# Kernel tuning notes

Measured on AMD Instinct MI355X. Metric: run time of the kernel, lower is better.

The kernel has to match this reference:

```python
import jax, jax.numpy as jnp
import numpy as np

H = 8        # num_heads
L = 2        # num_layers
F = 9        # num_fields
D = 128      # n_field_info
DH = D       # per-head depth = (D*H)//H
NB = 50      # n_base
EXCL = (0, 1, 2)  # fields excluded in FinalMerge (SelfAttention_Ex0, n_fields-3 inputs)
EPS = 1e-5


def _ln(x, g, b):
    m = jnp.mean(x, -1, keepdims=True)
    v = jnp.mean((x - m) ** 2, -1, keepdims=True)
    return (x - m) / jnp.sqrt(v + EPS) * g + b


def _forward(Y, Gin, posW1, posB1, posW2, posB2, posW3, posB3,
             Wq, bq, Wk, bk, Wv, bv, Wo, bo, lnG, lnB, fnG, fnB, poolW,
             uQW, uQB, uKW, uKB, uVW, uVB, mQW, mQB, mKW, mKB, mVW, mVB):
    B, S, _ = Y.shape
    pooled = []
    for f in range(F):  # per-field towers are structurally distinct (separate params)
        gy = jnp.concatenate([Y, Gin[:, :, f:f + 1]], axis=-1)        # [B,S,NB+1]
        h = jnp.tanh(gy @ posW1[f].T + posB1[f])
        h = jnp.tanh(h @ posW2[f].T + posB2[f])
        x = jax.nn.sigmoid(h @ posW3[f].T + posB3[f])                  # [B,S,D]
        for l in range(L):
            q = (x @ Wq[l, f].T + bq[l, f]).reshape(B, S, H, DH).transpose(0, 2, 1, 3)
            k = (x @ Wk[l, f].T + bk[l, f]).reshape(B, S, H, DH).transpose(0, 2, 1, 3)
            v = (x @ Wv[l, f].T + bv[l, f]).reshape(B, S, H, DH).transpose(0, 2, 1, 3)
            att = jax.nn.softmax(jnp.einsum('bhsd,bhtd->bhst', q, k) / jnp.sqrt(jnp.float32(DH)), axis=-1)
            wv = jnp.einsum('bhst,bhtd->bhsd', att, v).transpose(0, 2, 1, 3).reshape(B, S, H * DH)
            out = wv @ Wo[l, f].T + bo[l, f]
            x = _ln(x + out, lnG[l, f], lnB[l, f])   # residual + per-field LayerNorm
        x = _ln(x, fnG, fnB)                         # final_norm
        sc = jax.nn.softmax(x @ poolW[f][:, None], axis=1)             # GlobalAttentionPooling, [B,S,1]
        pooled.append(jnp.sum(x * sc, axis=1))                         # [B,D]
    U = jnp.stack(pooled, axis=-1)                                     # [B,D,F]

    unified = []
    for f in range(F):  # SelfAttention per target field
        Q = U @ uQW[f].T + uQB[f]                                      # [B,D,D]
        K = U @ uKW[f].T + uKB[f]
        V = U @ uVW[f].T + uVB[f]
        A = jax.nn.softmax(jnp.einsum('bik,bjk->bij', Q, K) / jnp.sqrt(jnp.float32(F)), axis=-1)
        o = jnp.einsum('bij,bjk->bik', A, V).mean(axis=-1)             # [B,D]
        o = o + (U[:, :, f] if f > 0 else U.mean(axis=-1))
        unified.append(o)
    Uu = jnp.stack(unified, axis=-1)                                   # [B,D,F]

    inc = [i for i in range(F) if i not in EXCL]
    Us = U[:, :, jnp.array(inc)]                                       # [B,D,F-3]
    Q = Us @ mQW.T + mQB
    K = Us @ mKW.T + mKB
    V = Us @ mVW.T + mVB
    A = jax.nn.softmax(jnp.einsum('bik,bjk->bij', Q, K) / jnp.sqrt(jnp.float32(F)), axis=-1)
    g = jnp.einsum('bij,bjk->bik', A, V).mean(axis=-1) + Us.mean(axis=-1)  # [B,D]
    return jnp.concatenate([Uu, g[:, :, None]], axis=-1)               # [B,D,F+1]


def setup_inputs() -> dict:
    key = jax.random.key(0)
    ks = iter(jax.random.split(key, 64))
    nrm = lambda shape, s=1.0: jax.random.normal(next(ks), shape, dtype=jnp.float32) * s
    B, S = 8, 512
    d = {}
    d['Y'] = nrm((B, S, NB))
    d['Gin'] = nrm((B, S, F))
    d['posW1'] = nrm((F, 50, NB + 1), 0.14); d['posB1'] = jnp.zeros((F, 50))
    d['posW2'] = nrm((F, 50, 50), 0.14);     d['posB2'] = jnp.zeros((F, 50))
    d['posW3'] = nrm((F, D, 50), 0.14);      d['posB3'] = jnp.zeros((F, D))
    d['Wq'] = nrm((L, F, H * DH, D), 0.09);  d['bq'] = jnp.zeros((L, F, H * DH))
    d['Wk'] = nrm((L, F, H * DH, D), 0.09);  d['bk'] = jnp.zeros((L, F, H * DH))
    d['Wv'] = nrm((L, F, H * DH, D), 0.09);  d['bv'] = jnp.zeros((L, F, H * DH))
    d['Wo'] = nrm((L, F, D, H * DH), 0.03);  d['bo'] = jnp.zeros((L, F, D))
    d['lnG'] = jnp.ones((L, F, D)); d['lnB'] = jnp.zeros((L, F, D))
    d['fnG'] = jnp.ones((D,));      d['fnB'] = jnp.zeros((D,))
    d['poolW'] = nrm((F, D))
    d['uQW'] = nrm((F, D, F), 0.33); d['uQB'] = jnp.zeros((F, D))
    d['uKW'] = nrm((F, D, F), 0.33); d['uKB'] = jnp.zeros((F, D))
    d['uVW'] = nrm((F, D, F), 0.33); d['uVB'] = jnp.zeros((F, D))
    d['mQW'] = nrm((D, F - 3), 0.4); d['mQB'] = jnp.zeros((D,))
    d['mKW'] = nrm((D, F - 3), 0.4); d['mKB'] = jnp.zeros((D,))
    d['mVW'] = nrm((D, F - 3), 0.4); d['mVB'] = jnp.zeros((D,))
    return d


def reference(Y, Gin, posW1, posB1, posW2, posB2, posW3, posB3,
              Wq, bq, Wk, bk, Wv, bv, Wo, bo, lnG, lnB, fnG, fnB, poolW,
              uQW, uQB, uKW, uKB, uVW, uVB, mQW, mQB, mKW, mKB, mVW, mVB):
    return _forward(Y, Gin, posW1, posB1, posW2, posB2, posW3, posB3,
                    Wq, bq, Wk, bk, Wv, bv, Wo, bo, lnG, lnB, fnG, fnB, poolW,
                    uQW, uQB, uKW, uKB, uVW, uVB, mQW, mQB, mKW, mKB, mVW, mVB)
```

## Files before the change

### kernel.cpp

```cpp
#include <hip/hip_runtime.h>
#include <hip/hip_bf16.h>

#define F_  9
#define B_  8
#define S_  512
#define H_  8
#define DH_ 128
#define D_  128
#define NB_ 50
#define BS_ 4096
#define PERBUF 4194304UL
#define WELEMS 2359296UL

typedef short bf16x8 __attribute__((ext_vector_type(8)));
typedef float f32x4  __attribute__((ext_vector_type(4)));
typedef unsigned int u32x4 __attribute__((ext_vector_type(4)));

static __device__ __forceinline__ unsigned short f2b(float f) {
    unsigned int u = __float_as_uint(f);
    unsigned int r = (u + 0x7FFFu + ((u >> 16) & 1u)) >> 16;
    return (unsigned short)r;
}
static __device__ __forceinline__ float b2f(unsigned short u) {
    return __uint_as_float(((unsigned int)u) << 16);
}
static __device__ __forceinline__ unsigned int cvtpk(float lo, float hi) {
    unsigned int r;
    asm("v_cvt_pk_bf16_f32 %0, %1, %2" : "=v"(r) : "v"(lo), "v"(hi));
    return r;
}

__global__ __launch_bounds__(256) void cvt_kernel(
    const float* __restrict__ in, unsigned short* __restrict__ out, int n)
{
    int i = (blockIdx.x * 256 + threadIdx.x) * 8;
    if (i + 8 <= n) {
        float4 a = *(const float4*)&in[i];
        float4 b = *(const float4*)&in[i + 4];
        ushort4 o0 = { f2b(a.x), f2b(a.y), f2b(a.z), f2b(a.w) };
        ushort4 o1 = { f2b(b.x), f2b(b.y), f2b(b.z), f2b(b.w) };
        *(ushort4*)&out[i]     = o0;
        *(ushort4*)&out[i + 4] = o1;
    }
}

__global__ __launch_bounds__(256) void posnet_kernel(
    const float* __restrict__ Y, const float* __restrict__ Gin,
    const float* __restrict__ W1g, const float* __restrict__ B1,
    const float* __restrict__ W2g, const float* __restrict__ B2,
    const float* __restrict__ W3g, const float* __restrict__ B3,
    float* __restrict__ xA, unsigned short* __restrict__ xAb)
{
    __shared__ float w1[50*51];
    __shared__ float w2[50*50];
    __shared__ float w3[128*50];
    __shared__ float b1[64], b2[64], b3[128];
    int f = blockIdx.z;
    int t = threadIdx.x;
    for (int i = t; i < 2550; i += 256) w1[i] = W1g[f*2550 + i];
    for (int i = t; i < 2500; i += 256) w2[i] = W2g[f*2500 + i];
    for (int i = t; i < 6400; i += 256) w3[i] = W3g[f*6400 + i];
    if (t < 50) { b1[t] = B1[f*50 + t]; b2[t] = B2[f*50 + t]; }
    if (t < 128) b3[t] = B3[f*128 + t];
    __syncthreads();

    int lane = t & 63, w = t >> 6;
    int row = blockIdx.x * 4 + w;

    float gy = 0.f;
    if (lane < 50)       gy = Y[(size_t)row*50 + lane];
    else if (lane == 50) gy = Gin[(size_t)row*F_ + f];

    float a1 = (lane < 50) ? b1[lane] : 0.f;
    for (int kk = 0; kk < 51; ++kk) {
        float g = __shfl(gy, kk);
        if (lane < 50) a1 += w1[lane*51 + kk] * g;
    }
    float h1 = tanhf(a1);

    float a2 = (lane < 50) ? b2[lane] : 0.f;
    for (int kk = 0; kk < 50; ++kk) {
        float hh = __shfl(h1, kk);
        if (lane < 50) a2 += w2[lane*50 + kk] * hh;
    }
    float h2 = tanhf(a2);

    float a30 = b3[lane], a31 = b3[64 + lane];
    for (int kk = 0; kk < 50; ++kk) {
        float hh = __shfl(h2, kk);
        a30 += w3[lane*50 + kk] * hh;
        a31 += w3[(64 + lane)*50 + kk] * hh;
    }
    float s0v = 1.f / (1.f + expf(-a30));
    float s1v = 1.f / (1.f + expf(-a31));
    size_t roff = ((size_t)f*BS_ + row)*128;
    xA[roff + lane]       = s0v;
    xA[roff + 64 + lane]  = s1v;
    xAb[roff + lane]      = f2b(s0v);
    xAb[roff + 64 + lane] = f2b(s1v);
}

__global__ __launch_bounds__(256) void qkv_mfma_kernel(
    const unsigned short* __restrict__ xb,
    const unsigned short* __restrict__ Wqb, const unsigned short* __restrict__ Wkb,
    const unsigned short* __restrict__ Wvb,
    const float* __restrict__ bq, const float* __restrict__ bk, const float* __restrict__ bv,
    unsigned short* __restrict__ qo, unsigned short* __restrict__ ko,
    unsigned int* __restrict__ vto, int l, int f0)
{
    int z = blockIdx.z;
    int fl = z / 3, which = z - fl*3;
    int f = f0 + fl;
    const unsigned short* W; const float* bias;
    if (which == 0)      { W = Wqb; bias = bq; }
    else if (which == 1) { W = Wkb; bias = bk; }
    else                 { W = Wvb; bias = bv; }
    W    += (size_t)(l*F_ + f) * 1024 * 128;
    bias += (size_t)(l*F_ + f) * 1024;

    int m0 = blockIdx.x * 128;
    int n0 = blockIdx.y * 128;
    int t = threadIdx.x, w = t >> 6, ln = t & 63, g = ln >> 4, c = ln & 15;
    int wr = w >> 1, wc = w & 1;

    const unsigned short* Ab = xb + ((size_t)f*BS_ + m0 + wr*64)*128;
    const unsigned short* Bb = W + (size_t)(n0 + wc*64)*128;

    f32x4 acc[4][4];
#pragma unroll
    for (int mi = 0; mi < 4; ++mi)
#pragma unroll
        for (int ni = 0; ni < 4; ++ni) acc[mi][ni] = (f32x4){0.f,0.f,0.f,0.f};

#pragma unroll
    for (int kt = 0; kt < 4; ++kt) {
        bf16x8 af[4], bfr[4];
#pragma unroll
        for (int mi = 0; mi < 4; ++mi)
            af[mi] = *(const bf16x8*)&Ab[(size_t)(mi*16 + c)*128 + kt*32 + g*8];
#pragma unroll
        for (int ni = 0; ni < 4; ++ni)
            bfr[ni] = *(const bf16x8*)&Bb[(size_t)(ni*16 + c)*128 + kt*32 + g*8];
#pragma unroll
        for (int mi = 0; mi < 4; ++mi)
#pragma unroll
            for (int ni = 0; ni < 4; ++ni)
                acc[mi][ni] = __builtin_amdgcn_mfma_f32_16x16x32_bf16(af[mi], bfr[ni], acc[mi][ni], 0, 0, 0);
    }

    int h = n0 >> 7;
    float bs_[4];
#pragma unroll
    for (int ni = 0; ni < 4; ++ni) bs_[ni] = bias[n0 + wc*64 + ni*16 + c];

    if (which < 2) {
        float qscale = (which == 0) ? 0.08838834764831845f : 1.0f;
        unsigned short* out = (which == 0 ? qo : ko) + (size_t)fl * PERBUF;
#pragma unroll
        for (int mi = 0; mi < 4; ++mi) {
#pragma unroll
            for (int r = 0; r < 4; ++r) {
                int m = m0 + wr*64 + mi*16 + 4*g + r;
                int b = m >> 9, s = m & 511;
                unsigned short* orow = out + (((size_t)(b*H_ + h))*S_ + s)*128;
#pragma unroll
                for (int ni = 0; ni < 4; ++ni)
                    orow[wc*64 + ni*16 + c] = f2b((acc[mi][ni][r] + bs_[ni]) * qscale);
            }
        }
    } else {
        unsigned int* vtf = vto + (size_t)fl * (PERBUF/2);
#pragma unroll
        for (int mi = 0; mi < 4; ++mi) {
            int mbase = m0 + wr*64 + mi*16 + 4*g;
            int b = mbase >> 9, sh = (mbase & 511) >> 1;
            unsigned int* vtp = vtf + ((size_t)(b*H_ + h))*32768;
#pragma unroll
            for (int ni = 0; ni < 4; ++ni) {
                int d = wc*64 + ni*16 + c;
                float bb_ = bs_[ni];
                unsigned int p01 = (unsigned int)f2b(acc[mi][ni][0] + bb_)
                                 | ((unsigned int)f2b(acc[mi][ni][1] + bb_) << 16);
                unsigned int p23 = (unsigned int)f2b(acc[mi][ni][2] + bb_)
                                 | ((unsigned int)f2b(acc[mi][ni][3] + bb_) << 16);
                vtp[(size_t)d*256 + sh]     = p01;
                vtp[(size_t)d*256 + sh + 1] = p23;
            }
        }
    }
}

__global__ __launch_bounds__(256) void attn_mfma_kernel(
    const unsigned short* __restrict__ q, const unsigned short* __restrict__ k,
    const unsigned int* __restrict__ vt, unsigned short* __restrict__ wv)
{
    int t = threadIdx.x;
    int w = t >> 6, ln = t & 63, g = ln >> 4, c = ln & 15;
    int bid = blockIdx.x;
    int group = bid >> 5, within = bid & 31;
    int i = within >> 3, hl = within & 7;
    int hIdx = group*8 + hl;
    int fl = hIdx >> 6, by = hIdx & 63;
    int q0 = i*128 + w*32;

    const unsigned short* qh = q + ((size_t)(fl*64 + by))*S_*128;
    const unsigned short* kh = k + ((size_t)(fl*64 + by))*S_*128;
    const unsigned int*  vth = vt + ((size_t)(fl*64 + by))*32768;
    int b = by >> 3, h = by & 7;
    unsigned short* wvh = wv + ((size_t)(fl*B_ + b))*S_*1024 + h*128;

    __shared__ alignas(16) unsigned short Ks[2][32][136];
    __shared__ alignas(16) unsigned int   Vs[2][128][20];

    int krow = t >> 4, kseg = t & 15;
    int vrow = t >> 2, vseg = t & 3;

    bf16x8 qf[2][4];
#pragma unroll
    for (int gq = 0; gq < 2; ++gq)
#pragma unroll
        for (int d0 = 0; d0 < 4; ++d0)
            qf[gq][d0] = *(const bf16x8*)&qh[(size_t)(q0 + gq*16 + c)*128 + d0*32 + g*8];

    f32x4 acc[2][8];
#pragma unroll
    for (int gq = 0; gq < 2; ++gq)
#pragma unroll
        for (int i2 = 0; i2 < 8; ++i2) acc[gq][i2] = (f32x4){0.f, 0.f, 0.f, 0.f};
    float mrow[2] = {-1e30f, -1e30f};
    float lrow[2] = {0.f, 0.f};

    int srcA = ((g & 1) << 5) + c;
    int srcB = srcA + 16;
    bool glow = (g < 2);

    uint4 kr0, kr1, vr0, vr1;
    {
        kr0 = *(const uint4*)&kh[(size_t)krow*128 + kseg*8];
        kr1 = *(const uint4*)&kh[(size_t)(krow + 16)*128 + kseg*8];
        vr0 = *(const uint4*)&vth[(size_t)vrow*256 + vseg*4];
        vr1 = *(const uint4*)&vth[(size_t)(vrow + 64)*256 + vseg*4];
        *(uint4*)&Ks[0][krow][kseg*8]      = kr0;
        *(uint4*)&Ks[0][krow + 16][kseg*8] = kr1;
        *(uint4*)&Vs[0][vrow][vseg*4]      = vr0;
        *(uint4*)&Vs[0][vrow + 64][vseg*4] = vr1;
    }
    __syncthreads();

    int cur = 0;
    for (int kt = 0; kt < 16; ++kt) {
        if (kt < 15) {
            const unsigned short* ks = kh + (size_t)(kt + 1)*32*128;
            const unsigned int*  vsp = vth + (kt + 1)*16;
            kr0 = *(const uint4*)&ks[(size_t)krow*128 + kseg*8];
            kr1 = *(const uint4*)&ks[(size_t)(krow + 16)*128 + kseg*8];
            vr0 = *(const uint4*)&vsp[(size_t)vrow*256 + vseg*4];
            vr1 = *(const uint4*)&vsp[(size_t)(vrow + 64)*256 + vseg*4];
        }

        f32x4 s[2][2];
        s[0][0] = (f32x4){0.f,0.f,0.f,0.f}; s[0][1] = (f32x4){0.f,0.f,0.f,0.f};
        s[1][0] = (f32x4){0.f,0.f,0.f,0.f}; s[1][1] = (f32x4){0.f,0.f,0.f,0.f};
        __builtin_amdgcn_s_setprio(1);
#pragma unroll
        for (int d0 = 0; d0 < 4; ++d0) {
            bf16x8 k0 = *(const bf16x8*)&Ks[cur][c][g*8 + d0*32];
            bf16x8 k1 = *(const bf16x8*)&Ks[cur][16 + c][g*8 + d0*32];
#pragma unroll
            for (int gq = 0; gq < 2; ++gq) {
                s[gq][0] = __builtin_amdgcn_mfma_f32_16x16x32_bf16(k0, qf[gq][d0], s[gq][0], 0, 0, 0);
                s[gq][1] = __builtin_amdgcn_mfma_f32_16x16x32_bf16(k1, qf[gq][d0], s[gq][1], 0, 0, 0);
            }
        }
        __builtin_amdgcn_s_setprio(0);

        float corr[2];
        bf16x8 pa[2];
        bool need = false;
#pragma unroll
        for (int gq = 0; gq < 2; ++gq) {
            float t0 = fmaxf(fmaxf(fmaxf(s[gq][0][0], s[gq][0][1]), fmaxf(s[gq][0][2], s[gq][0][3])),
                             fmaxf(fmaxf(s[gq][1][0], s[gq][1][1]), fmaxf(s[gq][1][2], s[gq][1][3])));
            t0 = fmaxf(t0, __shfl_xor(t0, 16));
            t0 = fmaxf(t0, __shfl_xor(t0, 32));
            float mo = mrow[gq];
            float mn = (t0 > mo + 8.f) ? t0 : mo;
            float co = __expf(mo - mn);
            corr[gq] = co;
            mrow[gq] = mn;
            float p00 = __expf(s[gq][0][0] - mn), p01 = __expf(s[gq][0][1] - mn);
            float p02 = __expf(s[gq][0][2] - mn), p03 = __expf(s[gq][0][3] - mn);
            float p10 = __expf(s[gq][1][0] - mn), p11 = __expf(s[gq][1][1] - mn);
            float p12 = __expf(s[gq][1][2] - mn), p13 = __expf(s[gq][1][3] - mn);
            float ps = ((p00 + p01) + (p02 + p03)) + ((p10 + p11) + (p12 + p13));
            ps += __shfl_xor(ps, 16);
            ps += __shfl_xor(ps, 32);
            lrow[gq] = lrow[gq]*co + ps;
            need = need || (co != 1.0f);

            unsigned int pk0 = cvtpk(p00, p01), pk1 = cvtpk(p02, p03);
            unsigned int pk2 = cvtpk(p10, p11), pk3 = cvtpk(p12, p13);
            unsigned int a0 = __shfl(pk0, srcA), a1 = __shfl(pk1, srcA);
            unsigned int b0 = __shfl(pk0, srcB), b1 = __shfl(pk1, srcB);
            unsigned int c0 = __shfl(pk2, srcA), c1 = __shfl(pk3, srcA);
            unsigned int d0_ = __shfl(pk2, srcB), d1_ = __shfl(pk3, srcB);
            u32x4 pu;
            pu[0] = glow ? a0 : c0;
            pu[1] = glow ? a1 : c1;
            pu[2] = glow ? b0 : d0_;
            pu[3] = glow ? b1 : d1_;
            pa[gq] = __builtin_bit_cast(bf16x8, pu);
        }

        if (__any(need)) {
#pragma unroll
            for (int gq = 0; gq < 2; ++gq) {
                float cr0 = __shfl(corr[gq], 4*g + 0);
                float cr1 = __shfl(corr[gq], 4*g + 1);
                float cr2 = __shfl(corr[gq], 4*g + 2);
                float cr3 = __shfl(corr[gq], 4*g + 3);
#pragma unroll
                for (int i2 = 0; i2 < 8; ++i2) {
                    f32x4 a = acc[gq][i2];
                    a[0] *= cr0; a[1] *= cr1; a[2] *= cr2; a[3] *= cr3;
                    acc[gq][i2] = a;
                }
            }
        }

        __builtin_amdgcn_s_setprio(1);
#pragma unroll
        for (int i2 = 0; i2 < 8; ++i2) {
            bf16x8 vf = *(const bf16x8*)&Vs[cur][i2*16 + c][g*4];
            acc[0][i2] = __builtin_amdgcn_mfma_f32_16x16x32_bf16(pa[0], vf, acc[0][i2], 0, 0, 0);
            acc[1][i2] = __builtin_amdgcn_mfma_f32_16x16x32_bf16(pa[1], vf, acc[1][i2], 0, 0, 0);
        }
        __builtin_amdgcn_s_setprio(0);

        if (kt < 15) {
            __syncthreads();
            int nxt = cur ^ 1;
            *(uint4*)&Ks[nxt][krow][kseg*8]      = kr0;
            *(uint4*)&Ks[nxt][krow + 16][kseg*8] = kr1;
            *(uint4*)&Vs[nxt][vrow][vseg*4]      = vr0;
            *(uint4*)&Vs[nxt][vrow + 64][vseg*4] = vr1;
            __syncthreads();
            cur = nxt;
        }
    }

#pragma unroll
    for (int gq = 0; gq < 2; ++gq) {
        float invq = 1.0f / lrow[gq];
        float iv0 = __shfl(invq, 4*g + 0);
        float iv1 = __shfl(invq, 4*g + 1);
        float iv2 = __shfl(invq, 4*g + 2);
        float iv3 = __shfl(invq, 4*g + 3);
#pragma unroll
        for (int i2 = 0; i2 < 8; ++i2) {
            unsigned short* wp = &wvh[(size_t)(q0 + gq*16 + 4*g)*1024 + i2*16 + c];
            wp[0]    = f2b(acc[gq][i2][0]*iv0);
            wp[1024] = f2b(acc[gq][i2][1]*iv1);
            wp[2048] = f2b(acc[gq][i2][2]*iv2);
            wp[3072] = f2b(acc[gq][i2][3]*iv3);
        }
    }
}

__global__ __launch_bounds__(256) void outproj_mfma_kernel(
    const unsigned short* __restrict__ wv, const unsigned short* __restrict__ Wob,
    const float* __restrict__ bo, const float* __restrict__ xin,
    float* __restrict__ xout, int l, int f0)
{
    int fl = blockIdx.z, f = f0 + fl;
    int m0 = blockIdx.x * 128;
    int t = threadIdx.x, w = t >> 6, ln = t & 63, g = ln >> 4, c = ln & 15;
    int wr = w >> 1, wc = w & 1;

    const unsigned short* Ab = wv + ((size_t)fl*BS_ + m0 + wr*64)*1024;
    const unsigned short* Bb = Wob + (size_t)(l*F_ + f)*128*1024 + (size_t)(wc*64)*1024;
    const float* bob = bo + (size_t)(l*F_ + f)*128;

    f32x4 acc[4][4];
#pragma unroll
    for (int mi = 0; mi < 4; ++mi)
#pragma unroll
        for (int ni = 0; ni < 4; ++ni) acc[mi][ni] = (f32x4){0.f,0.f,0.f,0.f};

#pragma unroll 4
    for (int kt = 0; kt < 32; ++kt) {
        bf16x8 af[4], bfr[4];
#pragma unroll
        for (int mi = 0; mi < 4; ++mi)
            af[mi] = *(const bf16x8*)&Ab[(size_t)(mi*16 + c)*1024 + kt*32 + g*8];
#pragma unroll
        for (int ni = 0; ni < 4; ++ni)
            bfr[ni] = *(const bf16x8*)&Bb[(size_t)(ni*16 + c)*1024 + kt*32 + g*8];
#pragma unroll
        for (int mi = 0; mi < 4; ++mi)
#pragma unroll
            for (int ni = 0; ni < 4; ++ni)
                acc[mi][ni] = __builtin_amdgcn_mfma_f32_16x16x32_bf16(af[mi], bfr[ni], acc[mi][ni], 0, 0, 0);
    }

    float bs_[4];
#pragma unroll
    for (int ni = 0; ni < 4; ++ni) bs_[ni] = bob[wc*64 + ni*16 + c];

#pragma unroll
    for (int mi = 0; mi < 4; ++mi) {
#pragma unroll
        for (int r = 0; r < 4; ++r) {
            int m = m0 + wr*64 + mi*16 + 4*g + r;
            const float* xr = xin + ((size_t)f*BS_ + m)*128;
            float* xo = xout + ((size_t)f*BS_ + m)*128;
#pragma unroll
            for (int ni = 0; ni < 4; ++ni) {
                int n = wc*64 + ni*16 + c;
                xo[n] = acc[mi][ni][r] + bs_[ni] + xr[n];
            }
        }
    }
}

__global__ __launch_bounds__(256) void ln_kernel(
    const float* __restrict__ xin, float* __restrict__ xout,
    unsigned short* __restrict__ xoutb,
    const float* __restrict__ g, const float* __restrict__ bb, int f0, int gstride)
{
    int t = threadIdx.x, lane = t & 63, w = t >> 6;
    int rowl = blockIdx.x * 4 + w;
    int fl = rowl >> 12;
    size_t row = (size_t)f0*BS_ + rowl;
    const float* xi = xin + row*128;
    float a = xi[lane], c = xi[64 + lane];
    float s = a + c;
#pragma unroll
    for (int off = 1; off < 64; off <<= 1) s += __shfl_xor(s, off);
    float mean = s * (1.0f/128.0f);
    float da = a - mean, dc = c - mean;
    float vs = da*da + dc*dc;
#pragma unroll
    for (int off = 1; off < 64; off <<= 1) vs += __shfl_xor(vs, off);
    float inv = rsqrtf(vs * (1.0f/128.0f) + 1e-5f);
    const float* gp = g + (size_t)fl*gstride;
    const float* bp = bb + (size_t)fl*gstride;
    float o0 = da*inv*gp[lane]      + bp[lane];
    float o1 = dc*inv*gp[64 + lane] + bp[64 + lane];
    float* xo = xout + row*128;
    xo[lane]      = o0;
    xo[64 + lane] = o1;
    xoutb[row*128 + lane]      = f2b(o0);
    xoutb[row*128 + 64 + lane] = f2b(o1);
}

__global__ __launch_bounds__(256) void pool_kernel(
    const float* __restrict__ xB, const float* __restrict__ poolW,
    float* __restrict__ U, int f0)
{
    int f = f0 + blockIdx.x, b = blockIdx.y;
    const float* xb = xB + ((size_t)f*BS_ + (size_t)b*S_)*128;
    const float* pw = poolW + f*128;
    __shared__ float sc[512];
    __shared__ float red[8];
    __shared__ float MS[2];
    __shared__ float pool2[256];
    int t = threadIdx.x, lane = t & 63, w = t >> 6;

    float p0 = pw[lane], p1 = pw[64 + lane];
    for (int s = w; s < 512; s += 4) {
        float a = xb[(size_t)s*128 + lane]*p0 + xb[(size_t)s*128 + 64 + lane]*p1;
#pragma unroll
        for (int off = 1; off < 64; off <<= 1) a += __shfl_xor(a, off);
        if (lane == 0) sc[s] = a;
    }
    __syncthreads();

    float m = -1e30f;
    for (int s = t; s < 512; s += 256) m = fmaxf(m, sc[s]);
#pragma unroll
    for (int off = 1; off < 64; off <<= 1) m = fmaxf(m, __shfl_xor(m, off));
    if (lane == 0) red[w] = m;
    __syncthreads();
    if (t == 0) MS[0] = fmaxf(fmaxf(red[0], red[1]), fmaxf(red[2], red[3]));
    __syncthreads();
    float M = MS[0];

    float ssum = 0.f;
    for (int s = t; s < 512; s += 256) { float e = expf(sc[s] - M); sc[s] = e; ssum += e; }
#pragma unroll
    for (int off = 1; off < 64; off <<= 1) ssum += __shfl_xor(ssum, off);
    if (lane == 0) red[4 + w] = ssum;
    __syncthreads();
    if (t == 0) MS[1] = red[4] + red[5] + red[6] + red[7];
    __syncthreads();
    float inv = 1.0f / MS[1];

    int d = t & 127, hh = t >> 7;
    float a = 0.f;
    for (int s = hh*256; s < hh*256 + 256; ++s) a += sc[s]*xb[(size_t)s*128 + d];
    pool2[t] = a;
    __syncthreads();
    if (t < 128) U[((size_t)b*128 + d)*F_ + f] = (pool2[t] + pool2[t + 128]) * inv;
}

__global__ __launch_bounds__(256) void unified_kernel(
    const float* __restrict__ U,
    const float* __restrict__ uQW, const float* __restrict__ uQB,
    const float* __restrict__ uKW, const float* __restrict__ uKB,
    const float* __restrict__ uVW, const float* __restrict__ uVB,
    float* __restrict__ outp)
{
    int f = blockIdx.x, b = blockIdx.y;
    __shared__ float Ub[128*9];
    __shared__ float Wj[128*9];
    __shared__ float zj[128];
    __shared__ float vm[128];
    __shared__ float Mm[81];
    __shared__ float wvm[9], bvec[9];
    __shared__ float cc_[2];
    int t = threadIdx.x;
    for (int i = t; i < 1152; i += 256) Ub[i] = U[(size_t)b*1152 + i];
    const float* qw = uQW + (size_t)f*1152;
    const float* kw = uKW + (size_t)f*1152;
    const float* vw = uVW + (size_t)f*1152;
    const float* qb = uQB + (size_t)f*128;
    const float* kb = uKB + (size_t)f*128;
    const float* vb = uVB + (size_t)f*128;

    if (t < 81) {
        int t1 = t/9, s1 = t%9; float a = 0.f;
        for (int kk = 0; kk < 128; ++kk) a += qw[kk*9 + t1]*kw[kk*9 + s1];
        Mm[t] = a;
    } else if (t < 90) {
        int s1 = t - 81; float a = 0.f;
        for (int kk = 0; kk < 128; ++kk) a += kw[kk*9 + s1]*qb[kk];
        bvec[s1] = a;
    } else if (t < 99) {
        int t1 = t - 90; float a = 0.f;
        for (int kk = 0; kk < 128; ++kk) a += vw[kk*9 + t1];
        wvm[t1] = a * (1.0f/128.0f);
    } else if (t == 99) {
        float a = 0.f, c2 = 0.f;
        for (int kk = 0; kk < 128; ++kk) { a += qb[kk]*kb[kk]; c2 += vb[kk]; }
        cc_[0] = a; cc_[1] = c2 * (1.0f/128.0f);
    }
    __syncthreads();

    if (t < 128) {
        int j = t;
        for (int t1 = 0; t1 < 9; ++t1) {
            float a = 0.f;
            for (int s1 = 0; s1 < 9; ++s1) a += Mm[t1*9 + s1]*Ub[j*9 + s1];
            Wj[j*9 + t1] = a;
        }
        float z = cc_[0], v2 = cc_[1];
        for (int s1 = 0; s1 < 9; ++s1) { z += bvec[s1]*Ub[j*9 + s1]; v2 += wvm[s1]*Ub[j*9 + s1]; }
        zj[j] = z; vm[j] = v2;
    }
    __syncthreads();

    int i = t >> 1, half = t & 1;
    float ui[9];
#pragma unroll
    for (int s1 = 0; s1 < 9; ++s1) ui[s1] = Ub[i*9 + s1];

    float mx = -1e30f;
    for (int jj = 0; jj < 64; ++jj) {
        int j = half*64 + jj;
        float a = zj[j];
#pragma unroll
        for (int s1 = 0; s1 < 9; ++s1) a += ui[s1]*Wj[j*9 + s1];
        mx = fmaxf(mx, a * (1.0f/3.0f));
    }
    mx = fmaxf(mx, __shfl_xor(mx, 1));
    float sum = 0.f, o = 0.f;
    for (int jj = 0; jj < 64; ++jj) {
        int j = half*64 + jj;
        float a = zj[j];
#pragma unroll
        for (int s1 = 0; s1 < 9; ++s1) a += ui[s1]*Wj[j*9 + s1];
        float p = expf(a * (1.0f/3.0f) - mx);
        sum += p; o += p*vm[j];
    }
    sum += __shfl_xor(sum, 1);
    o   += __shfl_xor(o, 1);
    if (half == 0) {
        float base;
        if (f > 0) base = ui[f];
        else { base = 0.f; for (int s1 = 0; s1 < 9; ++s1) base += ui[s1]; base *= (1.0f/9.0f); }
        outp[((size_t)b*128 + i)*10 + f] = o/sum + base;
    }
}

__global__ __launch_bounds__(256) void merge_kernel(
    const float* __restrict__ U,
    const float* __restrict__ mQW, const float* __restrict__ mQB,
    const float* __restrict__ mKW, const float* __restrict__ mKB,
    const float* __restrict__ mVW, const float* __restrict__ mVB,
    float* __restrict__ outp)
{
    int b = blockIdx.x;
    __shared__ float Us[128*6];
    __shared__ float Wj[128*6];
    __shared__ float zj[128];
    __shared__ float vm[128];
    __shared__ float Mm[36];
    __shared__ float wvm[6], bvec[6];
    __shared__ float cc_[2];
    int t = threadIdx.x;
    for (int i = t; i < 768; i += 256) {
        int j = i/6, tt = i - j*6;
        Us[i] = U[(size_t)b*1152 + j*9 + 3 + tt];
    }
    if (t < 36) {
        int t1 = t/6, s1 = t%6; float a = 0.f;
        for (int kk = 0; kk < 128; ++kk) a += mQW[kk*6 + t1]*mKW[kk*6 + s1];
        Mm[t] = a;
    } else if (t < 42) {
        int s1 = t - 36; float a = 0.f;
        for (int kk = 0; kk < 128; ++kk) a += mKW[kk*6 + s1]*mQB[kk];
        bvec[s1] = a;
    } else if (t < 48) {
        int t1 = t - 42; float a = 0.f;
        for (int kk = 0; kk < 128; ++kk) a += mVW[kk*6 + t1];
        wvm[t1] = a * (1.0f/128.0f);
    } else if (t == 48) {
        float a = 0.f, c2 = 0.f;
        for (int kk = 0; kk < 128; ++kk) { a += mQB[kk]*mKB[kk]; c2 += mVB[kk]; }
        cc_[0] = a; cc_[1] = c2 * (1.0f/128.0f);
    }
    __syncthreads();

    if (t < 128) {
        int j = t;
        for (int t1 = 0; t1 < 6; ++t1) {
            float a = 0.f;
            for (int s1 = 0; s1 < 6; ++s1) a += Mm[t1*6 + s1]*Us[j*6 + s1];
            Wj[j*6 + t1] = a;
        }
        float z = cc_[0], v2 = cc_[1];
        for (int s1 = 0; s1 < 6; ++s1) { z += bvec[s1]*Us[j*6 + s1]; v2 += wvm[s1]*Us[j*6 + s1]; }
        zj[j] = z; vm[j] = v2;
    }
    __syncthreads();

    int i = t >> 1, half = t & 1;
    float ui[6];
#pragma unroll
    for (int s1 = 0; s1 < 6; ++s1) ui[s1] = Us[i*6 + s1];

    float mx = -1e30f;
    for (int jj = 0; jj < 64; ++jj) {
        int j = half*64 + jj;
        float a = zj[j];
#pragma unroll
        for (int s1 = 0; s1 < 6; ++s1) a += ui[s1]*Wj[j*6 + s1];
        mx = fmaxf(mx, a * (1.0f/3.0f));
    }
    mx = fmaxf(mx, __shfl_xor(mx, 1));
    float sum = 0.f, o = 0.f;
    for (int jj = 0; jj < 64; ++jj) {
        int j = half*64 + jj;
        float a = zj[j];
#pragma unroll
        for (int s1 = 0; s1 < 6; ++s1) a += ui[s1]*Wj[j*6 + s1];
        float p = expf(a * (1.0f/3.0f) - mx);
        sum += p; o += p*vm[j];
    }
    sum += __shfl_xor(sum, 1);
    o   += __shfl_xor(o, 1);
    if (half == 0) {
        float base = 0.f;
        for (int s1 = 0; s1 < 6; ++s1) base += ui[s1];
        base *= (1.0f/6.0f);
        outp[((size_t)b*128 + i)*10 + 9] = o/sum + base;
    }
}

extern "C" void kernel_launch(void* const* d_in, const int* in_sizes, int n_in,
                              void* d_out, int out_size, void* d_ws, size_t ws_size,
                              hipStream_t stream)
{
    const float* Y     = (const float*)d_in[0];
    const float* Gin   = (const float*)d_in[1];
    const float* posW1 = (const float*)d_in[2];
    const float* posB1 = (const float*)d_in[3];
    const float* posW2 = (const float*)d_in[4];
    const float* posB2 = (const float*)d_in[5];
    const float* posW3 = (const float*)d_in[6];
    const float* posB3 = (const float*)d_in[7];
    const float* Wq    = (const float*)d_in[8];
    const float* bq    = (const float*)d_in[9];
    const float* Wk    = (const float*)d_in[10];
    const float* bk    = (const float*)d_in[11];
    const float* Wv    = (const float*)d_in[12];
    const float* bv    = (const float*)d_in[13];
    const float* Wo    = (const float*)d_in[14];
    const float* bo    = (const float*)d_in[15];
    const float* lnG   = (const float*)d_in[16];
    const float* lnB   = (const float*)d_in[17];
    const float* fnG   = (const float*)d_in[18];
    const float* fnB   = (const float*)d_in[19];
    const float* poolW = (const float*)d_in[20];
    const float* uQW   = (const float*)d_in[21];
    const float* uQB   = (const float*)d_in[22];
    const float* uKW   = (const float*)d_in[23];
    const float* uKB   = (const float*)d_in[24];
    const float* uVW   = (const float*)d_in[25];
    const float* uVB   = (const float*)d_in[26];
    const float* mQW   = (const float*)d_in[27];
    const float* mQB   = (const float*)d_in[28];
    const float* mKW   = (const float*)d_in[29];
    const float* mKB   = (const float*)d_in[30];
    const float* mVW   = (const float*)d_in[31];
    const float* mVB   = (const float*)d_in[32];

    const size_t xelems = (size_t)F_ * BS_ * 128;
    char* p = (char*)d_ws;
    float* xA   = (float*)p;               p += xelems*4;
    float* xB   = (float*)p;               p += xelems*4;
    float* Ubuf = (float*)p;               p += 16384*4;
    unsigned short* xAb = (unsigned short*)p; p += xelems*2;
    unsigned short* Wqb = (unsigned short*)p; p += WELEMS*2;
    unsigned short* Wkb = (unsigned short*)p; p += WELEMS*2;
    unsigned short* Wvb = (unsigned short*)p; p += WELEMS*2;
    unsigned short* Wob = (unsigned short*)p; p += WELEMS*2;
    size_t fixed_bytes = (size_t)(p - (char*)d_ws);

    size_t avail = (ws_size > fixed_bytes) ? (ws_size - fixed_bytes) : 0;
    size_t per_f = 8UL * PERBUF;
    int FC = (int)(avail / per_f);
    if (FC < 1) FC = 1;
    if (FC > F_) FC = F_;

    unsigned short* qb  = (unsigned short*)p;
    unsigned short* kb  = qb + (size_t)FC*PERBUF;
    unsigned short* wvb = kb + (size_t)FC*PERBUF;
    unsigned int*   vtb = (unsigned int*)(wvb + (size_t)FC*PERBUF);

    {
        int n = (int)WELEMS, grid = (n/8 + 255)/256;
        cvt_kernel<<<grid, 256, 0, stream>>>(Wq, Wqb, n);
        cvt_kernel<<<grid, 256, 0, stream>>>(Wk, Wkb, n);
        cvt_kernel<<<grid, 256, 0, stream>>>(Wv, Wvb, n);
        cvt_kernel<<<grid, 256, 0, stream>>>(Wo, Wob, n);
    }

    posnet_kernel<<<dim3(1024, 1, F_), 256, 0, stream>>>(
        Y, Gin, posW1, posB1, posW2, posB2, posW3, posB3, xA, xAb);

    for (int l = 0; l < 2; ++l) {
        for (int f0 = 0; f0 < F_; f0 += FC) {
            int fc = (F_ - f0) < FC ? (F_ - f0) : FC;
            qkv_mfma_kernel<<<dim3(32, 8, 3*fc), 256, 0, stream>>>(
                xAb, Wqb, Wkb, Wvb, bq, bk, bv, qb, kb, vtb, l, f0);
            attn_mfma_kernel<<<dim3(256*fc), 256, 0, stream>>>(qb, kb, vtb, wvb);
            outproj_mfma_kernel<<<dim3(32, 1, fc), 256, 0, stream>>>(
                wvb, Wob, bo, xA, xB, l, f0);
            ln_kernel<<<dim3(fc*1024), 256, 0, stream>>>(
                xB, xA, xAb, lnG + (size_t)(l*F_ + f0)*128, lnB + (size_t)(l*F_ + f0)*128, f0, 128);
        }
    }

    for (int f0 = 0; f0 < F_; f0 += FC) {
        int fc = (F_ - f0) < FC ? (F_ - f0) : FC;
        ln_kernel<<<dim3(fc*1024), 256, 0, stream>>>(xA, xB, xAb, fnG, fnB, f0, 0);
        pool_kernel<<<dim3(fc, 8), 256, 0, stream>>>(xB, poolW, Ubuf, f0);
    }

    unified_kernel<<<dim3(F_, B_), 256, 0, stream>>>(
        Ubuf, uQW, uQB, uKW, uKB, uVW, uVB, (float*)d_out);
    merge_kernel<<<dim3(B_), 256, 0, stream>>>(
        Ubuf, mQW, mQB, mKW, mKB, mVW, mVB, (float*)d_out);
}
```

Measured before the change: 1.174 ms.

## Restructure posnet to keep weights in registers and process 16 rows per wave

The position-net MLP now has each lane hold one weight row in registers and compute 16 rows per wave, with inputs staged in shared memory and read as float4. This replaces reloading every weight matrix into shared memory in each of 9216 tiny blocks, leaving 576 blocks with more reuse per weight. Separately, the four weight conversion launches are merged into one 2D-grid kernel to cut launch overhead. The register arrays (about 100 floats for the third layer plus accumulators) may raise register pressure and lower occupancy.

```diff
diff --git a/kernel.cpp b/kernel.cpp
--- a/kernel.cpp
+++ b/kernel.cpp
@@ -30,17 +30,27 @@
     return r;
 }
 
-__global__ __launch_bounds__(256) void cvt_kernel(
-    const float* __restrict__ in, unsigned short* __restrict__ out, int n)
-{
+__global__ __launch_bounds__(256) void cvt4_kernel(
+    const float* __restrict__ s0, const float* __restrict__ s1,
+    const float* __restrict__ s2, const float* __restrict__ s3,
+    unsigned short* __restrict__ d0, unsigned short* __restrict__ d1,
+    unsigned short* __restrict__ d2, unsigned short* __restrict__ d3, int n)
+{
+    const float* s; unsigned short* d;
+    switch (blockIdx.y) {
+        case 0: s = s0; d = d0; break;
+        case 1: s = s1; d = d1; break;
+        case 2: s = s2; d = d2; break;
+        default: s = s3; d = d3; break;
+    }
     int i = (blockIdx.x * 256 + threadIdx.x) * 8;
     if (i + 8 <= n) {
-        float4 a = *(const float4*)&in[i];
-        float4 b = *(const float4*)&in[i + 4];
+        float4 a = *(const float4*)&s[i];
+        float4 b = *(const float4*)&s[i + 4];
         ushort4 o0 = { f2b(a.x), f2b(a.y), f2b(a.z), f2b(a.w) };
         ushort4 o1 = { f2b(b.x), f2b(b.y), f2b(b.z), f2b(b.w) };
-        *(ushort4*)&out[i]     = o0;
-        *(ushort4*)&out[i + 4] = o1;
+        *(ushort4*)&d[i]     = o0;
+        *(ushort4*)&d[i + 4] = o1;
     }
 }
 
@@ -51,53 +61,112 @@
     const float* __restrict__ W3g, const float* __restrict__ B3,
     float* __restrict__ xA, unsigned short* __restrict__ xAb)
 {
-    __shared__ float w1[50*51];
-    __shared__ float w2[50*50];
-    __shared__ float w3[128*50];
-    __shared__ float b1[64], b2[64], b3[128];
-    int f = blockIdx.z;
-    int t = threadIdx.x;
-    for (int i = t; i < 2550; i += 256) w1[i] = W1g[f*2550 + i];
-    for (int i = t; i < 2500; i += 256) w2[i] = W2g[f*2500 + i];
-    for (int i = t; i < 6400; i += 256) w3[i] = W3g[f*6400 + i];
-    if (t < 50) { b1[t] = B1[f*50 + t]; b2[t] = B2[f*50 + t]; }
-    if (t < 128) b3[t] = B3[f*128 + t];
-    __syncthreads();
-
-    int lane = t & 63, w = t >> 6;
-    int row = blockIdx.x * 4 + w;
-
-    float gy = 0.f;
-    if (lane < 50)       gy = Y[(size_t)row*50 + lane];
-    else if (lane == 50) gy = Gin[(size_t)row*F_ + f];
-
-    float a1 = (lane < 50) ? b1[lane] : 0.f;
-    for (int kk = 0; kk < 51; ++kk) {
-        float g = __shfl(gy, kk);
-        if (lane < 50) a1 += w1[lane*51 + kk] * g;
-    }
-    float h1 = tanhf(a1);
-
-    float a2 = (lane < 50) ? b2[lane] : 0.f;
-    for (int kk = 0; kk < 50; ++kk) {
-        float hh = __shfl(h1, kk);
-        if (lane < 50) a2 += w2[lane*50 + kk] * hh;
-    }
-    float h2 = tanhf(a2);
-
-    float a30 = b3[lane], a31 = b3[64 + lane];
-    for (int kk = 0; kk < 50; ++kk) {
-        float hh = __shfl(h2, kk);
-        a30 += w3[lane*50 + kk] * hh;
-        a31 += w3[(64 + lane)*50 + kk] * hh;
-    }
-    float s0v = 1.f / (1.f + expf(-a30));
-    float s1v = 1.f / (1.f + expf(-a31));
-    size_t roff = ((size_t)f*BS_ + row)*128;
-    xA[roff + lane]       = s0v;
-    xA[roff + 64 + lane]  = s1v;
-    xAb[roff + lane]      = f2b(s0v);
-    xAb[roff + 64 + lane] = f2b(s1v);
+    __shared__ float gys[4][16][52];
+    __shared__ float hs[4][16][52];
+
+    int f = blockIdx.y;
+    int t = threadIdx.x, w = t >> 6, j = t & 63;
+    int rowbase = blockIdx.x * 64 + w * 16;
+
+#pragma unroll
+    for (int rr = 0; rr < 16; ++rr) {
+        int row = rowbase + rr;
+        if (j < 50)       gys[w][rr][j]  = Y[(size_t)row*50 + j];
+        else if (j == 50) gys[w][rr][50] = Gin[(size_t)row*F_ + f];
+    }
+
+    int jj = (j < 50) ? j : 0;
+    float acc0[16], acc1[16];
+
+    {
+        const float* wp = W1g + f*2550 + jj*51;
+        float wreg[51];
+#pragma unroll
+        for (int kk = 0; kk < 51; ++kk) wreg[kk] = wp[kk];
+        float bb = B1[f*50 + jj];
+#pragma unroll
+        for (int rr = 0; rr < 16; ++rr) acc0[rr] = bb;
+#pragma unroll
+        for (int k4 = 0; k4 < 48; k4 += 4) {
+#pragma unroll
+            for (int rr = 0; rr < 16; ++rr) {
+                float4 gv = *(const float4*)&gys[w][rr][k4];
+                acc0[rr] += wreg[k4]*gv.x + wreg[k4+1]*gv.y + wreg[k4+2]*gv.z + wreg[k4+3]*gv.w;
+            }
+        }
+#pragma unroll
+        for (int kk = 48; kk < 51; ++kk)
+#pragma unroll
+            for (int rr = 0; rr < 16; ++rr) acc0[rr] += wreg[kk]*gys[w][rr][kk];
+        if (j < 50) {
+#pragma unroll
+            for (int rr = 0; rr < 16; ++rr) hs[w][rr][j] = tanhf(acc0[rr]);
+        }
+    }
+
+    {
+        const float* wp = W2g + f*2500 + jj*50;
+        float wreg[50];
+#pragma unroll
+        for (int kk = 0; kk < 50; ++kk) wreg[kk] = wp[kk];
+        float bb = B2[f*50 + jj];
+#pragma unroll
+        for (int rr = 0; rr < 16; ++rr) acc0[rr] = bb;
+#pragma unroll
+        for (int k4 = 0; k4 < 48; k4 += 4) {
+#pragma unroll
+            for (int rr = 0; rr < 16; ++rr) {
+                float4 gv = *(const float4*)&hs[w][rr][k4];
+                acc0[rr] += wreg[k4]*gv.x + wreg[k4+1]*gv.y + wreg[k4+2]*gv.z + wreg[k4+3]*gv.w;
+            }
+        }
+#pragma unroll
+        for (int kk = 48; kk < 50; ++kk)
+#pragma unroll
+            for (int rr = 0; rr < 16; ++rr) acc0[rr] += wreg[kk]*hs[w][rr][kk];
+        if (j < 50) {
+#pragma unroll
+            for (int rr = 0; rr < 16; ++rr) gys[w][rr][j] = tanhf(acc0[rr]);
+        }
+    }
+
+    {
+        const float* wp0 = W3g + f*6400 + j*50;
+        const float* wp1 = wp0 + 64*50;
+        float wreg0[50], wreg1[50];
+#pragma unroll
+        for (int kk = 0; kk < 50; ++kk) { wreg0[kk] = wp0[kk]; wreg1[kk] = wp1[kk]; }
+        float b0 = B3[f*128 + j], b1v = B3[f*128 + 64 + j];
+#pragma unroll
+        for (int rr = 0; rr < 16; ++rr) { acc0[rr] = b0; acc1[rr] = b1v; }
+#pragma unroll
+        for (int k4 = 0; k4 < 48; k4 += 4) {
+#pragma unroll
+            for (int rr = 0; rr < 16; ++rr) {
+                float4 gv = *(const float4*)&gys[w][rr][k4];
+                acc0[rr] += wreg0[k4]*gv.x + wreg0[k4+1]*gv.y + wreg0[k4+2]*gv.z + wreg0[k4+3]*gv.w;
+                acc1[rr] += wreg1[k4]*gv.x + wreg1[k4+1]*gv.y + wreg1[k4+2]*gv.z + wreg1[k4+3]*gv.w;
+            }
+        }
+#pragma unroll
+        for (int kk = 48; kk < 50; ++kk)
+#pragma unroll
+            for (int rr = 0; rr < 16; ++rr) {
+                float gv = gys[w][rr][kk];
+                acc0[rr] += wreg0[kk]*gv;
+                acc1[rr] += wreg1[kk]*gv;
+            }
+#pragma unroll
+        for (int rr = 0; rr < 16; ++rr) {
+            float x0 = 1.f / (1.f + expf(-acc0[rr]));
+            float x1 = 1.f / (1.f + expf(-acc1[rr]));
+            size_t roff = ((size_t)f*BS_ + rowbase + rr)*128;
+            xA[roff + j]       = x0;
+            xA[roff + 64 + j]  = x1;
+            xAb[roff + j]      = f2b(x0);
+            xAb[roff + 64 + j] = f2b(x1);
+        }
+    }
 }
 
 __global__ __launch_bounds__(256) void qkv_mfma_kernel(
@@ -740,14 +809,12 @@
     unsigned int*   vtb = (unsigned int*)(wvb + (size_t)FC*PERBUF);
 
     {
-        int n = (int)WELEMS, grid = (n/8 + 255)/256;
-        cvt_kernel<<<grid, 256, 0, stream>>>(Wq, Wqb, n);
-        cvt_kernel<<<grid, 256, 0, stream>>>(Wk, Wkb, n);
-        cvt_kernel<<<grid, 256, 0, stream>>>(Wv, Wvb, n);
-        cvt_kernel<<<grid, 256, 0, stream>>>(Wo, Wob, n);
-    }
-
-    posnet_kernel<<<dim3(1024, 1, F_), 256, 0, stream>>>(
+        int n = (int)WELEMS, gx = (n/8 + 255)/256;
+        cvt4_kernel<<<dim3(gx, 4), 256, 0, stream>>>(
+            Wq, Wk, Wv, Wo, Wqb, Wkb, Wvb, Wob, n);
+    }
+
+    posnet_kernel<<<dim3(64, F_), 256, 0, stream>>>(
         Y, Gin, posW1, posB1, posW2, posB2, posW3, posB3, xA, xAb);
 
     for (int l = 0; l < 2; ++l) {
```

Result: slower. 1.313 ms (+11.8%).
